# Kernel tuning notes

Hardware: AMD Instinct MI355X
Metric: run time of the kernel (lower is better)

## Reference

```python
import jax, jax.numpy as jnp
import numpy as np

N_NODES = 50000
N_EDGES = 800000
IN_CH = 128
HEADS = 4
OUT_CH = 32
NEG_SLOPE = 0.2


def setup_inputs() -> dict:
    key = jax.random.key(0)
    ks = jax.random.split(key, 8)
    x = jax.random.normal(ks[0], (N_NODES, IN_CH), dtype=jnp.float32)
    # edges guaranteed to have no self-loops (module removes then re-adds them)
    tgt = jax.random.randint(ks[1], (N_EDGES,), 0, N_NODES)
    off = jax.random.randint(ks[2], (N_EDGES,), 1, N_NODES)
    src = (tgt + off) % N_NODES
    edge_index = jnp.stack([src, tgt]).astype(jnp.int64)
    glorot = lambda k, shp: jax.random.uniform(
        k, shp, jnp.float32, -1.0, 1.0) * np.sqrt(6.0 / (shp[-1] + shp[-2]))
    Wl = glorot(ks[3], (HEADS * OUT_CH, IN_CH))  # torch Linear weight [out,in]
    Wr = glorot(ks[4], (HEADS * OUT_CH, IN_CH))
    att = glorot(ks[5], (1, HEADS, OUT_CH))
    bl = jnp.zeros((HEADS * OUT_CH,), jnp.float32)
    br = jnp.zeros((HEADS * OUT_CH,), jnp.float32)
    bias = jnp.zeros((HEADS * OUT_CH,), jnp.float32)
    return {"x": x, "edge_index": edge_index, "Wl": Wl, "bl": bl,
            "Wr": Wr, "br": br, "att": att, "bias": bias}


def _forward(x, edge_index, Wl, bl, Wr, br, att, bias):
    H, C = HEADS, OUT_CH
    n = x.shape[0]
    x_l = (x @ Wl.T + bl).reshape(n, H, C)  # target projection
    x_r = (x @ Wr.T + br).reshape(n, H, C)  # source projection
    # add self-loops (inputs contain none by construction)
    loops = jnp.arange(n, dtype=edge_index.dtype)
    src = jnp.concatenate([edge_index[0], loops])
    tgt = jnp.concatenate([edge_index[1], loops])
    x_i = x_l[tgt]                     # [E', H, C]
    x_j = x_r[src]                     # [E', H, C]
    a_in = jax.nn.leaky_relu(x_i + x_j, NEG_SLOPE)
    alpha = jnp.einsum('ehc,ohc->eh', a_in, att)  # [E', H]
    # segment softmax over target nodes
    m = jax.ops.segment_max(alpha, tgt, num_segments=n)
    alpha = jnp.exp(alpha - jax.lax.stop_gradient(m)[tgt])
    denom = jax.ops.segment_sum(alpha, tgt, num_segments=n)
    alpha = alpha / denom[tgt]
    msgs = x_j * alpha[:, :, None]     # [E', H, C]
    out = jax.ops.segment_sum(msgs, tgt, num_segments=n)  # [N, H, C]
    out = out.reshape(n, H * C) + bias  # concat=True
    return out


def reference(x, edge_index, Wl, bl, Wr, br, att, bias):
    return _forward(x, edge_index, Wl, bl, Wr, br, att, bias)
```

## Files before the change

kernel.cpp:

```cpp
#include <hip/hip_runtime.h>
#include <hip/hip_bf16.h>
#include <stdint.h>

#define N_NODES 50000
#define N_EDGES 800000
#define IN_CH   128
#define NEG_SLOPE 0.2f

#define NBUCK   196
#define E1      4000
#define FILLB   200
#define BCAP    6144
#define BSTRIDE 24576
#define CAPR    48

#define E_PER 8
#define FILL_BLOCKS 391

typedef short short8 __attribute__((ext_vector_type(8)));
typedef float f32x4  __attribute__((ext_vector_type(4)));
typedef float f32x2  __attribute__((ext_vector_type(2)));

static __device__ __forceinline__ float bf_lo(uint32_t p) { return __uint_as_float(p << 16); }
static __device__ __forceinline__ float bf_hi(uint32_t p) { return __uint_as_float(p & 0xffff0000u); }
static __device__ __forceinline__ uint16_t f_to_bf(float f) {
    uint32_t u = __float_as_uint(f);
    u += 0x7fffu + ((u >> 16) & 1u);
    return (uint16_t)(u >> 16);
}

static __device__ __forceinline__ f32x2 lrelu2(f32x2 x) {
    f32x2 s = x * NEG_SLOPE;
    f32x2 r;
    r[0] = fmaxf(x[0], s[0]);
    r[1] = fmaxf(x[1], s[1]);
    return r;
}

#define DPPADD(x, ctrl) __uint_as_float(__builtin_amdgcn_update_dpp(0, __float_as_uint(x), ctrl, 0xf, 0xf, true))

static __device__ __forceinline__ void wswz_body(
    int t, const float* __restrict__ Wl, const float* __restrict__ Wr,
    __hip_bfloat16* __restrict__ wswz)
{
    int ct = t >> 8, rem = t & 255;
    int ch = rem >> 6, lane = rem & 63;
    int m = lane & 15, quad = lane >> 4;
    const float* W = (ct < 8) ? Wl : Wr;
    int o = ((ct & 7) << 4) + m;
    const float* src = W + (size_t)o * IN_CH + ch * 32 + quad * 8;
    short8 f;
#pragma unroll
    for (int j = 0; j < 8; ++j) f[j] = (short)f_to_bf(src[j]);
    *(short8*)((short*)wswz + (size_t)t * 8) = f;
}

template<bool XLBF>
static __device__ __forceinline__ void proj_body(
    int rowbase, int tid,
    const float* __restrict__ x, const __hip_bfloat16* __restrict__ wswz,
    const float* __restrict__ bl, const float* __restrict__ br,
    void* __restrict__ xl, __hip_bfloat16* __restrict__ xr)
{
    int lane = tid & 63;
    int widx = tid >> 6;
    int m = lane & 15;
    int quad = lane >> 4;

    short8 afrag[4];
    const float* xrow = x + (size_t)(rowbase + m) * IN_CH;
#pragma unroll
    for (int ch = 0; ch < 4; ++ch) {
        f32x4 p0 = *(const f32x4*)(xrow + ch * 32 + quad * 8);
        f32x4 p1 = *(const f32x4*)(xrow + ch * 32 + quad * 8 + 4);
        short8 f;
#pragma unroll
        for (int j = 0; j < 4; ++j) { f[j] = (short)f_to_bf(p0[j]); f[j + 4] = (short)f_to_bf(p1[j]); }
        afrag[ch] = f;
    }

    const short* wz = (const short*)wswz;
    const float* bv = (widx < 2) ? bl : br;
#pragma unroll
    for (int cc = 0; cc < 4; ++cc) {
        int ct = widx * 4 + cc;
        int o = ((ct & 7) << 4) + m;
        f32x4 acc = {0.f, 0.f, 0.f, 0.f};
#pragma unroll
        for (int ch = 0; ch < 4; ++ch) {
            short8 bfrag = *(const short8*)(wz + ((size_t)(ct * 4 + ch) * 64 + lane) * 8);
            acc = __builtin_amdgcn_mfma_f32_16x16x32_bf16(afrag[ch], bfrag, acc, 0, 0, 0);
        }
        float bias_v = bv[o];
        if (widx < 2) {
#pragma unroll
            for (int r = 0; r < 4; ++r) {
                size_t idx = (size_t)(rowbase + quad * 4 + r) * IN_CH + o;
                if constexpr (XLBF)
                    ((__hip_bfloat16*)xl)[idx] = __float2bfloat16(acc[r] + bias_v);
                else
                    ((float*)xl)[idx] = acc[r] + bias_v;
            }
        } else {
#pragma unroll
            for (int r = 0; r < 4; ++r)
                xr[(size_t)(rowbase + quad * 4 + r) * IN_CH + o] = __float2bfloat16(acc[r] + bias_v);
        }
    }
}

__global__ __launch_bounds__(256) void prep_kernel(
    const float* __restrict__ Wl, const float* __restrict__ Wr,
    __hip_bfloat16* __restrict__ wswz, int* __restrict__ z, int zn)
{
    int t = blockIdx.x * 256 + threadIdx.x;
    if (t < 4096) wswz_body(t, Wl, Wr, wswz);
    for (int i = t; i < zn; i += 64 * 256) z[i] = 0;
}

template<bool XLBF>
__global__ __launch_bounds__(256) void proj_fill(
    const float* __restrict__ x, const __hip_bfloat16* __restrict__ wswz,
    const float* __restrict__ bl, const float* __restrict__ br,
    void* __restrict__ xl, __hip_bfloat16* __restrict__ xr,
    const int* __restrict__ ei, uint32_t* __restrict__ bcnt,
    char* __restrict__ region)
{
    __shared__ uint32_t s_sorted[E1];
    __shared__ uint32_t s_hist[NBUCK], s_lstart[NBUCK], s_loc[NBUCK], s_gbase[NBUCK];
    __shared__ uint32_t s_T;

    if (blockIdx.x >= FILLB) {
        proj_body<XLBF>((blockIdx.x - FILLB) * 16, threadIdx.x, x, wswz, bl, br, xl, xr);
        return;
    }

    int tid = threadIdx.x;
    int fb = blockIdx.x;
    for (int i = tid; i < NBUCK; i += 256) s_hist[i] = 0;
    __syncthreads();

    const uint32_t* eiw = (const uint32_t*)ei;
    bool zlo = (eiw[2 * (tid & 63) + 1] == 0u);
    bool is64 = __popcll(__ballot(zlo)) >= 32;
    int e0 = fb * E1;

    for (int k = tid; k < E1; k += 256) {
        int e = e0 + k;
        int s = is64 ? (int)eiw[2 * (size_t)e] : ei[e];
        int t = is64 ? (int)eiw[2 * ((size_t)N_EDGES + e)] : ei[N_EDGES + e];
        if ((unsigned)s < N_NODES && (unsigned)t < N_NODES)
            atomicAdd(&s_hist[t >> 8], 1u);
    }
    __syncthreads();

    if (tid < NBUCK) s_gbase[tid] = atomicAdd(&bcnt[tid], s_hist[tid]);
    if (tid == 0) {
        uint32_t acc = 0;
        for (int i = 0; i < NBUCK; ++i) { s_lstart[i] = acc; acc += s_hist[i]; }
        s_T = acc;
    }
    __syncthreads();
    if (tid < NBUCK) s_loc[tid] = s_lstart[tid];
    __syncthreads();

    for (int k = tid; k < E1; k += 256) {
        int e = e0 + k;
        int s = is64 ? (int)eiw[2 * (size_t)e] : ei[e];
        int t = is64 ? (int)eiw[2 * ((size_t)N_EDGES + e)] : ei[N_EDGES + e];
        if ((unsigned)s < N_NODES && (unsigned)t < N_NODES) {
            uint32_t r = atomicAdd(&s_loc[t >> 8], 1u);
            s_sorted[r] = ((uint32_t)t << 16) | (uint32_t)s;
        }
    }
    __syncthreads();

    int T = (int)s_T;
    for (int k = tid; k < T; k += 256) {
        uint32_t v = s_sorted[k];
        uint32_t key = v >> 24;
        uint32_t g = s_gbase[key] + (uint32_t)k - s_lstart[key];
        if (g < BCAP)
            ((uint32_t*)(region + (size_t)key * BSTRIDE))[g] = v;
    }
}

__global__ __launch_bounds__(256) void csr_build(
    const uint32_t* __restrict__ bcnt, char* __restrict__ region,
    uint32_t* __restrict__ degs32)
{
    __shared__ uint16_t slab[256 * CAPR];
    __shared__ uint32_t lcnt[256];
    int b = blockIdx.x, tid = threadIdx.x;
    lcnt[tid] = 0;
    __syncthreads();

    uint32_t* reg = (uint32_t*)(region + (size_t)b * BSTRIDE);
    int M = min((int)bcnt[b], BCAP);
    for (int k = tid; k < M; k += 256) {
        uint32_t v = reg[k];
        int node = (int)((v >> 16) & 255u);
        uint32_t pos = atomicAdd(&lcnt[node], 1u);
        if (pos < CAPR) slab[node * CAPR + pos] = (uint16_t)(v & 0xffffu);
    }
    __syncthreads();

    const uint32_t* sw = (const uint32_t*)slab;
    for (int j = tid; j < (256 * CAPR / 2); j += 256) reg[j] = sw[j];
    if (tid < 64) {
        uint32_t p = 0;
#pragma unroll
        for (int q = 0; q < 4; ++q) {
            uint32_t d = min(lcnt[tid * 4 + q], (uint32_t)CAPR);
            p |= d << (q * 8);
        }
        degs32[b * 64 + tid] = p;
    }
}

__global__ __launch_bounds__(256) void fill_kernel(
    const int* __restrict__ ei, int cap,
    int* __restrict__ cnt, uint16_t* __restrict__ csr)
{
    const uint32_t* eiw = (const uint32_t*)ei;
    bool z = (eiw[2 * (threadIdx.x & 63) + 1] == 0u);
    bool is64 = __popcll(__ballot(z)) >= 32;

    int tid = blockIdx.x * 256 + threadIdx.x;
    int e0 = tid * E_PER;
    if (e0 >= N_EDGES) return;

    int src[E_PER], tgt[E_PER];
    if (is64) {
        const int4* ps = (const int4*)(eiw + 2 * (size_t)e0);
        const int4* pt = (const int4*)(eiw + 2 * ((size_t)N_EDGES + e0));
#pragma unroll
        for (int k = 0; k < 4; ++k) {
            int4 s = ps[k], t = pt[k];
            src[2 * k] = s.x; src[2 * k + 1] = s.z;
            tgt[2 * k] = t.x; tgt[2 * k + 1] = t.z;
        }
    } else {
        const int4* ps = (const int4*)(ei + e0);
        const int4* pt = (const int4*)(ei + N_EDGES + e0);
#pragma unroll
        for (int k = 0; k < 2; ++k) {
            int4 s = ps[k], t = pt[k];
            src[4 * k] = s.x; src[4 * k + 1] = s.y; src[4 * k + 2] = s.z; src[4 * k + 3] = s.w;
            tgt[4 * k] = t.x; tgt[4 * k + 1] = t.y; tgt[4 * k + 2] = t.z; tgt[4 * k + 3] = t.w;
        }
    }

    int pos[E_PER];
#pragma unroll
    for (int k = 0; k < E_PER; ++k) {
        bool ok = (unsigned)src[k] < N_NODES && (unsigned)tgt[k] < N_NODES;
        pos[k] = ok ? atomicAdd(&cnt[tgt[k]], 1) : cap;
    }
#pragma unroll
    for (int k = 0; k < E_PER; ++k)
        if (pos[k] < cap) csr[(size_t)tgt[k] * cap + pos[k]] = (uint16_t)src[k];
}

__global__ __launch_bounds__(256) void proj_kernel(
    const float* __restrict__ x, const __hip_bfloat16* __restrict__ wswz,
    const float* __restrict__ bl, const float* __restrict__ br,
    float* __restrict__ xl, __hip_bfloat16* __restrict__ xr)
{
    proj_body<false>(blockIdx.x * 16, threadIdx.x, x, wswz, bl, br, xl, xr);
}

__global__ __launch_bounds__(256) void agg_kernel(
    const __hip_bfloat16* __restrict__ xr,
    const char* __restrict__ qb, int qbf,
    const char* __restrict__ degbase, int degpacked,
    const uint16_t* __restrict__ csr, int ldcsr, int cap,
    const float* __restrict__ att, const float* __restrict__ bias,
    float* out)
{
    int n = blockIdx.x * 4 + (threadIdx.x >> 6);
    if (n >= N_NODES) return;
    int lane = threadIdx.x & 63;
    int lpos = lane & 31;
    bool isB = lane >= 32;
    uint32_t voff = (uint32_t)lpos * 8u;

    const char* xrb = (const char*)xr;

    f32x2 q01, q23;
    if (qbf) {
        uint2 qa = *(const uint2*)(qb + (size_t)n * 256 + voff);
        q01[0] = bf_lo(qa.x); q01[1] = bf_hi(qa.x);
        q23[0] = bf_lo(qa.y); q23[1] = bf_hi(qa.y);
    } else {
        f32x4 qv4 = *(const f32x4*)((const float*)qb + (size_t)n * IN_CH + lpos * 4);
        q01[0] = qv4[0]; q01[1] = qv4[1];
        q23[0] = qv4[2]; q23[1] = qv4[3];
    }
    f32x4 av4 = *(const f32x4*)(att + lpos * 4);
    f32x4 bv4 = *(const f32x4*)(bias + lpos * 4);
    const float L2E = 1.44269504088896f;
    f32x2 a01; a01[0] = av4[0] * L2E; a01[1] = av4[1] * L2E;
    f32x2 a23; a23[0] = av4[2] * L2E; a23[1] = av4[3] * L2E;

    int deg;
    if (degpacked) {
        uint32_t pk = ((const uint32_t*)degbase)[n >> 2];
        deg = (int)((pk >> ((n & 3) * 8)) & 255u);
    } else {
        deg = ((const int*)degbase)[n];
    }
    deg = min(deg, cap);
    deg = min(deg, 63);

    const uint16_t* lst = csr + (size_t)n * ldcsr;
    int idxreg = (int)lst[min(max(lane - 1, 0), cap - 1)];
    idxreg = (lane == 0) ? n : idxreg;
    idxreg <<= 8;

    int last = deg;
    int FP   = (deg + 1) >> 1;
    int ODD  = (deg + 1) & 1;

    float lsum = 0.f;
    f32x2 acc0 = {0.f, 0.f}, acc1 = {0.f, 0.f};

#define PAIR_LOAD(p, udst) { \
        int sa_ = __builtin_amdgcn_readlane(idxreg, min(2 * (p), last)); \
        int sb_ = __builtin_amdgcn_readlane(idxreg, min(2 * (p) + 1, last)); \
        uint32_t vs_ = (uint32_t)(isB ? sb_ : sa_); \
        udst = *(const uint2*)(xrb + vs_ + voff); \
    }

#define PAIR_EVAL(u, MASKED) { \
        f32x2 c0_, c1_; \
        c0_[0] = bf_lo((u).x); c0_[1] = bf_hi((u).x); \
        c1_[0] = bf_lo((u).y); c1_[1] = bf_hi((u).y); \
        f32x2 r0_ = lrelu2(q01 + c0_) * a01; \
        f32x2 r1_ = lrelu2(q23 + c1_) * a23; \
        float t_ = (r0_[0] + r0_[1]) + (r1_[0] + r1_[1]); \
        t_ += DPPADD(t_, 0xB1);    \
        t_ += DPPADD(t_, 0x4E);    \
        t_ += DPPADD(t_, 0x141);   \
        float w_ = __builtin_amdgcn_exp2f(t_); \
        if (MASKED) w_ = isB ? 0.f : w_; \
        lsum += w_; \
        acc0 += w_ * c0_; \
        acc1 += w_ * c1_; \
    }

    uint2 u0, u1;
    PAIR_LOAD(0, u0);
    PAIR_LOAD(1, u1);
    for (int p = 0; p < FP; ++p) {
        uint2 u2;
        PAIR_LOAD(p + 2, u2);
        PAIR_EVAL(u0, false);
        u0 = u1; u1 = u2;
    }
    if (ODD) {
        PAIR_EVAL(u0, true);
    }

    lsum    += __shfl_xor(lsum,    32);
    acc0[0] += __shfl_xor(acc0[0], 32);
    acc0[1] += __shfl_xor(acc0[1], 32);
    acc1[0] += __shfl_xor(acc1[0], 32);
    acc1[1] += __shfl_xor(acc1[1], 32);

    float inv = 1.f / lsum;
    if (lane < 32) {
        f32x4 ov;
        ov[0] = acc0[0] * inv + bv4[0];
        ov[1] = acc0[1] * inv + bv4[1];
        ov[2] = acc1[0] * inv + bv4[2];
        ov[3] = acc1[1] * inv + bv4[3];
        *(f32x4*)(out + (size_t)n * IN_CH + lpos * 4) = ov;
    }
#undef PAIR_LOAD
#undef PAIR_EVAL
}

extern "C" void kernel_launch(void* const* d_in, const int* in_sizes, int n_in,
                              void* d_out, int out_size, void* d_ws, size_t ws_size,
                              hipStream_t stream) {
    const float* x    = (const float*)d_in[0];
    const int*   ei   = (const int*)d_in[1];
    const float* Wl   = (const float*)d_in[2];
    const float* bl   = (const float*)d_in[3];
    const float* Wr   = (const float*)d_in[4];
    const float* br   = (const float*)d_in[5];
    const float* att  = (const float*)d_in[6];
    const float* bias = (const float*)d_in[7];
    float* out = (float*)d_out;

    char* ws = (char*)d_ws;
    __hip_bfloat16* xr = (__hip_bfloat16*)(ws);

    const size_t XL_OFF   = 12800000;
    const size_t WSWZ_OFF = 25600000;
    const size_t DEGS_OFF = 25665536;
    const size_t BCNT_OFF = 25715712;
    const size_t REG_OFF  = 25716736;
    const size_t NEED     = REG_OFF + (size_t)NBUCK * BSTRIDE;

    if (ws_size >= NEED) {
        __hip_bfloat16* xl   = (__hip_bfloat16*)(ws + XL_OFF);
        __hip_bfloat16* wswz = (__hip_bfloat16*)(ws + WSWZ_OFF);
        uint32_t* degs   = (uint32_t*)(ws + DEGS_OFF);
        uint32_t* bcnt   = (uint32_t*)(ws + BCNT_OFF);
        char*     region = ws + REG_OFF;

        prep_kernel<<<64, 256, 0, stream>>>(Wl, Wr, wswz, (int*)bcnt, NBUCK);
        proj_fill<true><<<FILLB + N_NODES / 16, 256, 0, stream>>>(
            x, wswz, bl, br, (void*)xl, xr, ei, bcnt, region);
        csr_build<<<NBUCK, 256, 0, stream>>>(bcnt, region, degs);
        agg_kernel<<<N_NODES / 4, 256, 0, stream>>>(
            xr, (const char*)xl, 1, (const char*)degs, 1,
            (const uint16_t*)region, CAPR, CAPR, att, bias, out);
    } else {
        const size_t LG_WSWZ = 12800000;
        const size_t LG_CNT  = 12865536;
        const size_t CSR_BASE = 13065536;
        __hip_bfloat16* wswz = (__hip_bfloat16*)(ws + LG_WSWZ);
        int*      cnt = (int*)(ws + LG_CNT);
        uint16_t* csr = (uint16_t*)(ws + CSR_BASE);
        long long avail = (ws_size > CSR_BASE) ? (long long)(ws_size - CSR_BASE) : 0;
        int cap = (int)(avail / ((long long)N_NODES * 2));
        if (cap > 64) cap = 64;
        if (cap < 1)  cap = 1;

        prep_kernel<<<64, 256, 0, stream>>>(Wl, Wr, wswz, cnt, N_NODES);
        fill_kernel<<<FILL_BLOCKS, 256, 0, stream>>>(ei, cap, cnt, csr);
        proj_kernel<<<N_NODES / 16, 256, 0, stream>>>(x, wswz, bl, br, out, xr);
        agg_kernel<<<N_NODES / 4, 256, 0, stream>>>(
            xr, (const char*)out, 0, (const char*)cnt, 0,
            csr, cap, cap, att, bias, out);
    }
}
```

Before: 164.0 us.

## Project 32 rows per block to reuse weight fragments; deepen aggregation prefetch

The projection part of proj_fill now handles 32 node rows per block instead of 16. Each weight B-fragment load feeds two MFMAs, which halves weight traffic per row and halves the number of projection blocks. The aggregation loop also prefetches three edge pairs ahead instead of two to hide gather latency better. The cost is more registers per thread and a tail guard for the last partial tile.

```diff
diff --git a/kernel.cpp b/kernel.cpp
--- a/kernel.cpp
+++ b/kernel.cpp
@@ -13,6 +13,7 @@
 #define BCAP    6144
 #define BSTRIDE 24576
 #define CAPR    48
+#define PROJ32B 1563
 
 #define E_PER 8
 #define FILL_BLOCKS 391
@@ -109,6 +110,70 @@
     }
 }
 
+static __device__ __forceinline__ void proj_body32(
+    int rowbase, int tid,
+    const float* __restrict__ x, const __hip_bfloat16* __restrict__ wswz,
+    const float* __restrict__ bl, const float* __restrict__ br,
+    __hip_bfloat16* __restrict__ xl, __hip_bfloat16* __restrict__ xr)
+{
+    int lane = tid & 63;
+    int widx = tid >> 6;
+    int m = lane & 15;
+    int quad = lane >> 4;
+    bool t1 = (rowbase + 16 < N_NODES);
+
+    short8 af0[4], af1[4];
+    const float* xrow0 = x + (size_t)(rowbase + m) * IN_CH;
+#pragma unroll
+    for (int ch = 0; ch < 4; ++ch) {
+        f32x4 p0 = *(const f32x4*)(xrow0 + ch * 32 + quad * 8);
+        f32x4 p1 = *(const f32x4*)(xrow0 + ch * 32 + quad * 8 + 4);
+        short8 f;
+#pragma unroll
+        for (int j = 0; j < 4; ++j) { f[j] = (short)f_to_bf(p0[j]); f[j + 4] = (short)f_to_bf(p1[j]); }
+        af0[ch] = f;
+    }
+    if (t1) {
+        const float* xrow1 = x + (size_t)(rowbase + 16 + m) * IN_CH;
+#pragma unroll
+        for (int ch = 0; ch < 4; ++ch) {
+            f32x4 p0 = *(const f32x4*)(xrow1 + ch * 32 + quad * 8);
+            f32x4 p1 = *(const f32x4*)(xrow1 + ch * 32 + quad * 8 + 4);
+            short8 f;
+#pragma unroll
+            for (int j = 0; j < 4; ++j) { f[j] = (short)f_to_bf(p0[j]); f[j + 4] = (short)f_to_bf(p1[j]); }
+            af1[ch] = f;
+        }
+    }
+
+    const short* wz = (const short*)wswz;
+    const float* bv = (widx < 2) ? bl : br;
+#pragma unroll
+    for (int cc = 0; cc < 4; ++cc) {
+        int ct = widx * 4 + cc;
+        int o = ((ct & 7) << 4) + m;
+        f32x4 acc0 = {0.f, 0.f, 0.f, 0.f};
+        f32x4 acc1 = {0.f, 0.f, 0.f, 0.f};
+#pragma unroll
+        for (int ch = 0; ch < 4; ++ch) {
+            short8 bfrag = *(const short8*)(wz + ((size_t)(ct * 4 + ch) * 64 + lane) * 8);
+            acc0 = __builtin_amdgcn_mfma_f32_16x16x32_bf16(af0[ch], bfrag, acc0, 0, 0, 0);
+            if (t1)
+                acc1 = __builtin_amdgcn_mfma_f32_16x16x32_bf16(af1[ch], bfrag, acc1, 0, 0, 0);
+        }
+        float bias_v = bv[o];
+        __hip_bfloat16* dst = (widx < 2) ? xl : xr;
+#pragma unroll
+        for (int r = 0; r < 4; ++r)
+            dst[(size_t)(rowbase + quad * 4 + r) * IN_CH + o] = __float2bfloat16(acc0[r] + bias_v);
+        if (t1) {
+#pragma unroll
+            for (int r = 0; r < 4; ++r)
+                dst[(size_t)(rowbase + 16 + quad * 4 + r) * IN_CH + o] = __float2bfloat16(acc1[r] + bias_v);
+        }
+    }
+}
+
 __global__ __launch_bounds__(256) void prep_kernel(
     const float* __restrict__ Wl, const float* __restrict__ Wr,
     __hip_bfloat16* __restrict__ wswz, int* __restrict__ z, int zn)
@@ -118,11 +183,10 @@
     for (int i = t; i < zn; i += 64 * 256) z[i] = 0;
 }
 
-template<bool XLBF>
 __global__ __launch_bounds__(256) void proj_fill(
     const float* __restrict__ x, const __hip_bfloat16* __restrict__ wswz,
     const float* __restrict__ bl, const float* __restrict__ br,
-    void* __restrict__ xl, __hip_bfloat16* __restrict__ xr,
+    __hip_bfloat16* __restrict__ xl, __hip_bfloat16* __restrict__ xr,
     const int* __restrict__ ei, uint32_t* __restrict__ bcnt,
     char* __restrict__ region)
 {
@@ -131,7 +195,7 @@
     __shared__ uint32_t s_T;
 
     if (blockIdx.x >= FILLB) {
-        proj_body<XLBF>((blockIdx.x - FILLB) * 16, threadIdx.x, x, wswz, bl, br, xl, xr);
+        proj_body32((blockIdx.x - FILLB) * 32, threadIdx.x, x, wswz, bl, br, xl, xr);
         return;
     }
 
@@ -349,14 +413,15 @@
         acc1 += w_ * c1_; \
     }
 
-    uint2 u0, u1;
+    uint2 u0, u1, u2;
     PAIR_LOAD(0, u0);
     PAIR_LOAD(1, u1);
+    PAIR_LOAD(2, u2);
     for (int p = 0; p < FP; ++p) {
-        uint2 u2;
-        PAIR_LOAD(p + 2, u2);
+        uint2 u3;
+        PAIR_LOAD(p + 3, u3);
         PAIR_EVAL(u0, false);
-        u0 = u1; u1 = u2;
+        u0 = u1; u1 = u2; u2 = u3;
     }
     if (ODD) {
         PAIR_EVAL(u0, true);
@@ -412,8 +477,8 @@
         char*     region = ws + REG_OFF;
 
         prep_kernel<<<64, 256, 0, stream>>>(Wl, Wr, wswz, (int*)bcnt, NBUCK);
-        proj_fill<true><<<FILLB + N_NODES / 16, 256, 0, stream>>>(
-            x, wswz, bl, br, (void*)xl, xr, ei, bcnt, region);
+        proj_fill<<<FILLB + PROJ32B, 256, 0, stream>>>(
+            x, wswz, bl, br, xl, xr, ei, bcnt, region);
         csr_build<<<NBUCK, 256, 0, stream>>>(bcnt, region, degs);
         agg_kernel<<<N_NODES / 4, 256, 0, stream>>>(
             xr, (const char*)xl, 1, (const char*)degs, 1,
```

New measurement: 163.8 us. About the same (-0.1%).
